# Performance work log

Hardware: AMD Instinct MI355X
Metric: run time of the kernel (lower is better)

Reference implementation:

```python
import jax, jax.numpy as jnp
import numpy as np

EPS = 1e-12

def _l2n(x):
    # torch F.normalize(p=2, dim=0): x / max(||x||_2, eps)
    return x / jnp.maximum(jnp.linalg.norm(x), EPS)

def _gru_cell(x, h, Wi, Wh, bi, bh):
    # torch GRU cell math; Wi:(3H,Din), Wh:(3H,H)
    gi = Wi @ x + bi
    gh = Wh @ h + bh
    i_r, i_z, i_n = jnp.split(gi, 3)
    h_r, h_z, h_n = jnp.split(gh, 3)
    r = jax.nn.sigmoid(i_r + h_r)
    z = jax.nn.sigmoid(i_z + h_z)
    n = jnp.tanh(i_n + r * h_n)
    return (1.0 - z) * n + z * h

def setup_inputs() -> dict:
    key = jax.random.key(0)
    ks = jax.random.split(key, 20)
    m, n, T = 10, 10, 100
    H1, H2, HID = 1600, 400, 2000
    D_in, D_out = 2 * m + n, m * n
    f32 = jnp.float32
    inp = {
        'y': jax.random.normal(ks[0], (n, T), f32),
        'm1x_0': jax.random.normal(ks[1], (m,), f32),
        'F': jax.random.normal(ks[2], (m, m), f32) * 0.1,
        'Hm': jax.random.normal(ks[3], (n, m), f32) * 0.1,
        'h0': jax.random.normal(ks[4], (2, HID), f32),
        'W1': jax.random.normal(ks[5], (H1, D_in), f32) * 0.05,
        'b1': jax.random.normal(ks[6], (H1,), f32) * 0.05,
        'Wi0': jax.random.normal(ks[7], (3 * HID, H1), f32) * 0.02,
        'Wh0': jax.random.normal(ks[8], (3 * HID, HID), f32) * 0.02,
        'bi0': jax.random.normal(ks[9], (3 * HID,), f32) * 0.02,
        'bh0': jax.random.normal(ks[10], (3 * HID,), f32) * 0.02,
        'Wi1': jax.random.normal(ks[11], (3 * HID, HID), f32) * 0.02,
        'Wh1': jax.random.normal(ks[12], (3 * HID, HID), f32) * 0.02,
        'bi1': jax.random.normal(ks[13], (3 * HID,), f32) * 0.02,
        'bh1': jax.random.normal(ks[14], (3 * HID,), f32) * 0.02,
        'W2': jax.random.normal(ks[15], (H2, HID), f32) * 0.02,
        'b2': jax.random.normal(ks[16], (H2,), f32) * 0.02,
        'W3': jax.random.normal(ks[17], (D_out, H2), f32) * 0.01,
        'b3': jax.random.normal(ks[18], (D_out,), f32) * 0.01,
    }
    return inp

def reference(y, m1x_0, F, Hm, h0, W1, b1, Wi0, Wh0, bi0, bh0,
              Wi1, Wh1, bi1, bh1, W2, b2, W3, b3):
    n, T = y.shape
    m = m1x_0.shape[0]
    # first step uses obs_process_0 = h(f(m1x_0)) as y_previous surrogate
    y_prev0 = Hm @ (F @ m1x_0)
    carry0 = (m1x_0, jnp.zeros_like(m1x_0), m1x_0, y_prev0, h0[0], h0[1])

    def step(carry, yt):
        post, prev_post, prev_prior, y_prev, h1, h2 = carry
        prior = F @ post              # step_prior
        m1y = Hm @ prior
        f1 = _l2n(yt - y_prev)        # innovation diff feature
        f3 = _l2n(post - prev_post)   # posterior update feature
        f4 = _l2n(post - prev_prior)  # residual feature
        kin = jnp.concatenate([f1, f3, f4])  # (2m+n,)
        a = jax.nn.relu(W1 @ kin + b1)
        h1n = _gru_cell(a, h1, Wi0, Wh0, bi0, bh0)
        h2n = _gru_cell(h1n, h2, Wi1, Wh1, bi1, bh1)
        g = jax.nn.relu(W2 @ h2n + b2)
        KG = (W3 @ g + b3).reshape(m, n)
        dy = yt - m1y
        new_post = prior + KG @ dy
        return (new_post, post, prior, yt, h1n, h2n), new_post

    _, xs = jax.lax.scan(step, carry0, y.T)  # xs: (T, m)
    return xs.T  # (m, T)
```

## Files before the change

### kernel.cpp

```cpp
#include <hip/hip_runtime.h>
#include <math.h>

#define NB 256
#define NT 1024
#define NW 16
#define TT 100
#define MM 10
#define NN 10
#define HID 2000
#define H1 1600
#define H2 400
#define G3 6000
#define KP 2048
#define RPB 24

#define SCOPE_AGENT __HIP_MEMORY_SCOPE_AGENT

typedef _Float16 h2v __attribute__((ext_vector_type(2)));

__device__ __forceinline__ float sigf(float x) { return 1.f / (1.f + __expf(-x)); }
__device__ __forceinline__ float tanhfast(float x) { return 2.f / (1.f + __expf(-2.f * x)) - 1.f; }

__device__ __forceinline__ float ld_coh(const float* p) {
  return __hip_atomic_load(p, __ATOMIC_RELAXED, SCOPE_AGENT);
}
__device__ __forceinline__ void st_coh(float* p, float v) {
  __hip_atomic_store(p, v, __ATOMIC_RELAXED, SCOPE_AGENT);
}
__device__ __forceinline__ float2 ld_coh2(const float* p) {
  unsigned long long v = __hip_atomic_load((const unsigned long long*)p,
                                           __ATOMIC_RELAXED, SCOPE_AGENT);
  union { unsigned long long u; float2 f; } c; c.u = v; return c.f;
}
__device__ __forceinline__ void stage_coh(const float* __restrict__ src,
                                          float* __restrict__ dst, int n, int tid) {
  const int n2 = n >> 1;
  for (int j = tid; j < n2; j += NT) {
    float2 v = ld_coh2(src + 2 * j);
    dst[2 * j]     = v.x;
    dst[2 * j + 1] = v.y;
  }
}

__device__ __forceinline__ void gridbar(unsigned* flags, unsigned* release,
                                        unsigned ep, int tid, int blk) {
  __syncthreads();
  if (tid == 0)
    __hip_atomic_store(flags + blk * 16, ep, __ATOMIC_RELAXED, SCOPE_AGENT);
  if (blk == 0) {
    if (tid < NB) {
      while (__hip_atomic_load(flags + tid * 16, __ATOMIC_RELAXED, SCOPE_AGENT) < ep)
        __builtin_amdgcn_s_sleep(1);
    }
    __syncthreads();
    if (tid == 0)
      __hip_atomic_store(release, ep, __ATOMIC_RELAXED, SCOPE_AGENT);
  } else {
    if (tid == 0) {
      while (__hip_atomic_load(release, __ATOMIC_RELAXED, SCOPE_AGENT) < ep)
        __builtin_amdgcn_s_sleep(1);
    }
  }
  __syncthreads();
}

template<int K>
__device__ __forceinline__ float rowdotT(const float* __restrict__ row,
                                         const float* __restrict__ x, int ln) {
  constexpr int NFULL = K / 256;
  constexpr int REM   = K - NFULL * 256;
  const int base = ln * 4;
  float4 w[NFULL + (REM ? 1 : 0)];
  #pragma unroll
  for (int i = 0; i < NFULL; ++i)
    w[i] = *reinterpret_cast<const float4*>(row + base + i * 256);
  bool tail = false;
  if constexpr (REM != 0) {
    tail = (base + NFULL * 256 + 3 < K);
    if (tail) w[NFULL] = *reinterpret_cast<const float4*>(row + base + NFULL * 256);
  }
  float acc = 0.f;
  #pragma unroll
  for (int i = 0; i < NFULL; ++i) {
    const float4 xv = *reinterpret_cast<const float4*>(x + base + i * 256);
    acc = fmaf(w[i].x, xv.x, acc);
    acc = fmaf(w[i].y, xv.y, acc);
    acc = fmaf(w[i].z, xv.z, acc);
    acc = fmaf(w[i].w, xv.w, acc);
  }
  if constexpr (REM != 0) {
    if (tail) {
      const float4 xv = *reinterpret_cast<const float4*>(x + base + NFULL * 256);
      acc = fmaf(w[NFULL].x, xv.x, acc);
      acc = fmaf(w[NFULL].y, xv.y, acc);
      acc = fmaf(w[NFULL].z, xv.z, acc);
      acc = fmaf(w[NFULL].w, xv.w, acc);
    }
  }
  #pragma unroll
  for (int off = 32; off; off >>= 1) acc += __shfl_xor(acc, off, 64);
  return acc;
}

__device__ __forceinline__ void sweep24(const _Float16* __restrict__ W,
                                        const float* __restrict__ bias,
                                        int row0, int nrows,
                                        const _Float16* __restrict__ xh,
                                        float* __restrict__ outw,
                                        bool relu,
                                        int wv, int ln, int tid, float* red)
{
  const _Float16* wp = W + (size_t)row0 * KP + wv * 3072 + ln * 8;
  uint4 w[6];
  #pragma unroll
  for (int c = 0; c < 6; ++c)
    w[c] = *reinterpret_cast<const uint4*>(wp + c * 512);
  float a0 = 0.f, a1 = 0.f;
  const int first = (3 * wv) >> 1;
  #pragma unroll
  for (int c = 0; c < 6; ++c) {
    const int flat = wv * 3072 + c * 512;
    const int sel  = (flat >> 11) - first;
    const int col  = (flat & (KP - 1)) + ln * 8;
    const uint4 xv = *reinterpret_cast<const uint4*>(xh + col);
    union { uint4 u; h2v h[4]; } wu, xu;
    wu.u = w[c]; xu.u = xv;
    float acc = sel ? a1 : a0;
    #pragma unroll
    for (int q = 0; q < 4; ++q)
      acc = __builtin_amdgcn_fdot2(wu.h[q], xu.h[q], acc, false);
    if (sel) a1 = acc; else a0 = acc;
  }
  #pragma unroll
  for (int off = 32; off; off >>= 1) {
    a0 += __shfl_xor(a0, off, 64);
    a1 += __shfl_xor(a1, off, 64);
  }
  __syncthreads();
  if (ln == 0) { red[wv * 2] = a0; red[wv * 2 + 1] = a1; }
  __syncthreads();
  if (tid < nrows) {
    const int k = tid / 3, m = tid % 3;
    float v = (m == 0) ? red[4 * k]
            : (m == 1) ? red[4 * k + 1] + red[4 * k + 2]
                       : red[4 * k + 3];
    v += bias[row0 + tid];
    if (relu) v = fmaxf(v, 0.f);
    st_coh(outw + row0 + tid, v);
  }
}

__global__ __launch_bounds__(256)
void convh(const float* __restrict__ src, _Float16* __restrict__ dst,
           int rows, int K, int padrows) {
  const size_t total = (size_t)padrows * KP;
  for (size_t i = (size_t)blockIdx.x * blockDim.x + threadIdx.x; i < total;
       i += (size_t)gridDim.x * blockDim.x) {
    const int r = (int)(i >> 11), c = (int)(i & (KP - 1));
    float v = (r < rows && c < K) ? src[(size_t)r * K + c] : 0.f;
    dst[i] = (_Float16)v;
  }
}

__global__ __launch_bounds__(NT)
void knet_f16(const float* __restrict__ y, const float* __restrict__ m1x0,
              const float* __restrict__ F, const float* __restrict__ Hm,
              const float* __restrict__ h0,
              const float* __restrict__ W1, const float* __restrict__ b1,
              const float* __restrict__ Wi0, const float* __restrict__ Wh0,
              const float* __restrict__ bi0, const float* __restrict__ bh0,
              const float* __restrict__ Wi1, const float* __restrict__ Wh1,
              const float* __restrict__ bi1, const float* __restrict__ bh1,
              const float* __restrict__ W2, const float* __restrict__ b2,
              const float* __restrict__ W3, const float* __restrict__ b3,
              float* __restrict__ out, float* __restrict__ ws)
{
  const int blk = blockIdx.x, tid = threadIdx.x;
  const int wv = tid >> 6, ln = tid & 63;

  float* a_ws   = ws;
  float* gi0_ws = ws + 1600;
  float* gh0_ws = ws + 7600;
  float* gi1_ws = ws + 13600;
  float* gh1_ws = ws + 19600;
  float* g_ws   = ws + 25600;
  unsigned* flags   = (unsigned*)(ws + 26624);
  unsigned* release = flags + NB * 16;

  const _Float16* whbase = (const _Float16*)((const char*)ws + 131072);
  const _Float16* Wi0h = whbase;
  const _Float16* Wh0h = whbase + (size_t)G3 * KP;
  const _Float16* Wi1h = whbase + (size_t)2 * G3 * KP;
  const _Float16* Wh1h = whbase + (size_t)3 * G3 * KP;
  const _Float16* W2h  = whbase + (size_t)4 * G3 * KP;

  __shared__ __align__(16) _Float16 ah[KP];
  __shared__ __align__(16) _Float16 h1h[KP];
  __shared__ __align__(16) _Float16 h2h[KP];
  __shared__ __align__(16) float h1l[HID];
  __shared__ __align__(16) float h2l[HID];
  __shared__ __align__(16) float xs[416];
  __shared__ float red[32];
  __shared__ float post_s[MM], prevpost_s[MM], prevprior_s[MM], prior_s[MM];
  __shared__ float dy_s[NN], yprev_s[NN], tmp_s[MM];
  __shared__ float d1_s[NN], d3_s[MM], d4_s[MM];
  __shared__ float kin_s[32], nrm_s[3];
  __shared__ float v_s[MM * NN], np_s[MM];

  for (int j = tid; j < HID; j += NT) {
    float v1 = h0[j], v2 = h0[HID + j];
    h1l[j] = v1; h2l[j] = v2;
    h1h[j] = (_Float16)v1; h2h[j] = (_Float16)v2;
  }
  for (int j = HID + tid; j < KP; j += NT) { h1h[j] = (_Float16)0.f; h2h[j] = (_Float16)0.f; }
  for (int j = H1 + tid; j < KP; j += NT) ah[j] = (_Float16)0.f;
  __syncthreads();

  unsigned ep = 0;

  for (int t = 0; t < TT; ++t) {
    if (blk == NB - 1) {
      if (t > 0) {
        stage_coh(g_ws, xs, H2, tid);
        __syncthreads();
        for (int r = wv; r < MM * NN; r += NW) {
          float acc = rowdotT<H2>(W3 + (size_t)r * H2, xs, ln);
          if (ln == 0) v_s[r] = acc + b3[r];
        }
        __syncthreads();
        if (tid < MM) {
          float np = prior_s[tid];
          #pragma unroll
          for (int j = 0; j < NN; ++j) np = fmaf(v_s[tid * NN + j], dy_s[j], np);
          out[tid * TT + (t - 1)] = np;
          np_s[tid] = np;
        }
        __syncthreads();
        if (tid < MM) {
          prevpost_s[tid]  = post_s[tid];
          prevprior_s[tid] = prior_s[tid];
          post_s[tid]      = np_s[tid];
        }
        __syncthreads();
      } else {
        if (tid < MM) {
          post_s[tid]      = m1x0[tid];
          prevpost_s[tid]  = 0.f;
          prevprior_s[tid] = m1x0[tid];
          float tv = 0.f;
          for (int j = 0; j < MM; ++j) tv = fmaf(F[tid * MM + j], m1x0[j], tv);
          tmp_s[tid] = tv;
        }
        __syncthreads();
        if (tid < NN) {
          float yp = 0.f;
          for (int j = 0; j < MM; ++j) yp = fmaf(Hm[tid * MM + j], tmp_s[j], yp);
          yprev_s[tid] = yp;
        }
        __syncthreads();
      }
      if (tid < MM) {
        float pr = 0.f;
        for (int j = 0; j < MM; ++j) pr = fmaf(F[tid * MM + j], post_s[j], pr);
        prior_s[tid] = pr;
      }
      __syncthreads();
      if (tid < NN) {
        float my = 0.f;
        for (int j = 0; j < MM; ++j) my = fmaf(Hm[tid * MM + j], prior_s[j], my);
        float yt = y[tid * TT + t];
        dy_s[tid] = yt - my;
        d1_s[tid] = yt - ((t == 0) ? yprev_s[tid] : y[tid * TT + (t - 1)]);
        d3_s[tid] = post_s[tid] - prevpost_s[tid];
        d4_s[tid] = post_s[tid] - prevprior_s[tid];
      }
      __syncthreads();
      if (tid == 0) {
        float n1 = 0.f, n3 = 0.f, n4 = 0.f;
        for (int j = 0; j < NN; ++j) n1 += d1_s[j] * d1_s[j];
        for (int j = 0; j < MM; ++j) { n3 += d3_s[j] * d3_s[j]; n4 += d4_s[j] * d4_s[j]; }
        nrm_s[0] = fmaxf(sqrtf(n1), 1e-12f);
        nrm_s[1] = fmaxf(sqrtf(n3), 1e-12f);
        nrm_s[2] = fmaxf(sqrtf(n4), 1e-12f);
      }
      __syncthreads();
      if (tid < NN) kin_s[tid] = d1_s[tid] / nrm_s[0];
      if (tid < MM) {
        kin_s[NN + tid]      = d3_s[tid] / nrm_s[1];
        kin_s[NN + MM + tid] = d4_s[tid] / nrm_s[2];
      }
      __syncthreads();
      for (int r = tid; r < H1; r += NT) {
        float acc = b1[r];
        const float* row = W1 + (size_t)r * 30;
        #pragma unroll
        for (int k = 0; k < 30; ++k) acc = fmaf(row[k], kin_s[k], acc);
        st_coh(a_ws + r, fmaxf(acc, 0.f));
      }
    } else if (blk < 250) {
      sweep24(Wh1h, bh1, RPB * blk, RPB, h2h, gh1_ws, false, wv, ln, tid, red);
      if (t == 0)
        sweep24(Wh0h, bh0, RPB * blk, RPB, h1h, gh0_ws, false, wv, ln, tid, red);
    } else {
      sweep24(Wh0h, bh0, RPB * (blk - 250), RPB, h1h, gh0_ws, false, wv, ln, tid, red);
    }
    ++ep; gridbar(flags, release, ep, tid, blk);

    if (blk < 250) {
      const int n2 = H1 >> 1;
      for (int j = tid; j < n2; j += NT) {
        float2 v = ld_coh2(a_ws + 2 * j);
        ah[2 * j]     = (_Float16)v.x;
        ah[2 * j + 1] = (_Float16)v.y;
      }
      __syncthreads();
      sweep24(Wi0h, bi0, RPB * blk, RPB, ah, gi0_ws, false, wv, ln, tid, red);
    } else {
      sweep24(Wh0h, bh0, RPB * (blk - 245), RPB, h1h, gh0_ws, false, wv, ln, tid, red);
    }
    ++ep; gridbar(flags, release, ep, tid, blk);

    {
      for (int j = tid; j < HID / 2; j += NT) {
        float2 ir = ld_coh2(gi0_ws + 2 * j),            hr = ld_coh2(gh0_ws + 2 * j);
        float2 iz = ld_coh2(gi0_ws + HID + 2 * j),      hz = ld_coh2(gh0_ws + HID + 2 * j);
        float2 in_ = ld_coh2(gi0_ws + 2 * HID + 2 * j), hn = ld_coh2(gh0_ws + 2 * HID + 2 * j);
        float r0 = sigf(ir.x + hr.x), r1 = sigf(ir.y + hr.y);
        float z0 = sigf(iz.x + hz.x), z1 = sigf(iz.y + hz.y);
        float n0 = tanhfast(in_.x + r0 * hn.x), n1 = tanhfast(in_.y + r1 * hn.y);
        float o0 = (1.f - z0) * n0 + z0 * h1l[2 * j];
        float o1 = (1.f - z1) * n1 + z1 * h1l[2 * j + 1];
        h1l[2 * j] = o0; h1l[2 * j + 1] = o1;
        h1h[2 * j] = (_Float16)o0; h1h[2 * j + 1] = (_Float16)o1;
      }
      __syncthreads();
      if (blk < 250)
        sweep24(Wi1h, bi1, RPB * blk, RPB, h1h, gi1_ws, false, wv, ln, tid, red);
    }
    ++ep; gridbar(flags, release, ep, tid, blk);

    {
      for (int j = tid; j < HID / 2; j += NT) {
        float2 ir = ld_coh2(gi1_ws + 2 * j),            hr = ld_coh2(gh1_ws + 2 * j);
        float2 iz = ld_coh2(gi1_ws + HID + 2 * j),      hz = ld_coh2(gh1_ws + HID + 2 * j);
        float2 in_ = ld_coh2(gi1_ws + 2 * HID + 2 * j), hn = ld_coh2(gh1_ws + 2 * HID + 2 * j);
        float r0 = sigf(ir.x + hr.x), r1 = sigf(ir.y + hr.y);
        float z0 = sigf(iz.x + hz.x), z1 = sigf(iz.y + hz.y);
        float n0 = tanhfast(in_.x + r0 * hn.x), n1 = tanhfast(in_.y + r1 * hn.y);
        float o0 = (1.f - z0) * n0 + z0 * h2l[2 * j];
        float o1 = (1.f - z1) * n1 + z1 * h2l[2 * j + 1];
        h2l[2 * j] = o0; h2l[2 * j + 1] = o1;
        h2h[2 * j] = (_Float16)o0; h2h[2 * j + 1] = (_Float16)o1;
      }
      __syncthreads();
      if (blk < 239) {
        sweep24(Wh0h, bh0, RPB * (blk + 11), RPB, h1h, gh0_ws, false, wv, ln, tid, red);
      } else {
        const int task = blk - 239;
        const int row0 = RPB * task;
        const int nr = (H2 - row0 < RPB) ? (H2 - row0) : RPB;
        sweep24(W2h, b2, row0, nr, h2h, g_ws, true, wv, ln, tid, red);
      }
    }
    ++ep; gridbar(flags, release, ep, tid, blk);
  }

  if (blk == NB - 1) {
    stage_coh(g_ws, xs, H2, tid);
    __syncthreads();
    for (int r = wv; r < MM * NN; r += NW) {
      float acc = rowdotT<H2>(W3 + (size_t)r * H2, xs, ln);
      if (ln == 0) v_s[r] = acc + b3[r];
    }
    __syncthreads();
    if (tid < MM) {
      float np = prior_s[tid];
      #pragma unroll
      for (int j = 0; j < NN; ++j) np = fmaf(v_s[tid * NN + j], dy_s[j], np);
      out[tid * TT + (TT - 1)] = np;
    }
  }
}

__global__ __launch_bounds__(NT)
void knet_f32(const float* __restrict__ y, const float* __restrict__ m1x0,
              const float* __restrict__ F, const float* __restrict__ Hm,
              const float* __restrict__ h0,
              const float* __restrict__ W1, const float* __restrict__ b1,
              const float* __restrict__ Wi0, const float* __restrict__ Wh0,
              const float* __restrict__ bi0, const float* __restrict__ bh0,
              const float* __restrict__ Wi1, const float* __restrict__ Wh1,
              const float* __restrict__ bi1, const float* __restrict__ bh1,
              const float* __restrict__ W2, const float* __restrict__ b2,
              const float* __restrict__ W3, const float* __restrict__ b3,
              float* __restrict__ out, float* __restrict__ ws)
{
  const int blk = blockIdx.x, tid = threadIdx.x;
  const int wv = tid >> 6, ln = tid & 63;

  float* a_ws   = ws;
  float* gi0_ws = ws + 1600;
  float* gh0_ws = ws + 7600;
  float* gi1_ws = ws + 13600;
  float* gh1_ws = ws + 19600;
  float* g_ws   = ws + 25600;
  unsigned* flags   = (unsigned*)(ws + 26624);
  unsigned* release = flags + NB * 16;

  __shared__ __align__(16) float xs[1664];
  __shared__ __align__(16) float h1l[HID];
  __shared__ __align__(16) float h2l[HID];
  __shared__ float post_s[MM], prevpost_s[MM], prevprior_s[MM], prior_s[MM];
  __shared__ float dy_s[NN], yprev_s[NN], tmp_s[MM];
  __shared__ float d1_s[NN], d3_s[MM], d4_s[MM];
  __shared__ float kin_s[32], nrm_s[3];
  __shared__ float v_s[MM * NN], np_s[MM];

  for (int j = tid; j < HID; j += NT) { h1l[j] = h0[j]; h2l[j] = h0[HID + j]; }
  __syncthreads();

  unsigned ep = 0;

  for (int t = 0; t < TT; ++t) {
    if (blk == NB - 1) {
      if (t > 0) {
        stage_coh(g_ws, xs, H2, tid);
        __syncthreads();
        for (int r = wv; r < MM * NN; r += NW) {
          float acc = rowdotT<H2>(W3 + (size_t)r * H2, xs, ln);
          if (ln == 0) v_s[r] = acc + b3[r];
        }
        __syncthreads();
        if (tid < MM) {
          float np = prior_s[tid];
          #pragma unroll
          for (int j = 0; j < NN; ++j) np = fmaf(v_s[tid * NN + j], dy_s[j], np);
          out[tid * TT + (t - 1)] = np;
          np_s[tid] = np;
        }
        __syncthreads();
        if (tid < MM) {
          prevpost_s[tid]  = post_s[tid];
          prevprior_s[tid] = prior_s[tid];
          post_s[tid]      = np_s[tid];
        }
        __syncthreads();
      } else {
        if (tid < MM) {
          post_s[tid]      = m1x0[tid];
          prevpost_s[tid]  = 0.f;
          prevprior_s[tid] = m1x0[tid];
          float tv = 0.f;
          for (int j = 0; j < MM; ++j) tv = fmaf(F[tid * MM + j], m1x0[j], tv);
          tmp_s[tid] = tv;
        }
        __syncthreads();
        if (tid < NN) {
          float yp = 0.f;
          for (int j = 0; j < MM; ++j) yp = fmaf(Hm[tid * MM + j], tmp_s[j], yp);
          yprev_s[tid] = yp;
        }
        __syncthreads();
      }
      if (tid < MM) {
        float pr = 0.f;
        for (int j = 0; j < MM; ++j) pr = fmaf(F[tid * MM + j], post_s[j], pr);
        prior_s[tid] = pr;
      }
      __syncthreads();
      if (tid < NN) {
        float my = 0.f;
        for (int j = 0; j < MM; ++j) my = fmaf(Hm[tid * MM + j], prior_s[j], my);
        float yt = y[tid * TT + t];
        dy_s[tid] = yt - my;
        d1_s[tid] = yt - ((t == 0) ? yprev_s[tid] : y[tid * TT + (t - 1)]);
        d3_s[tid] = post_s[tid] - prevpost_s[tid];
        d4_s[tid] = post_s[tid] - prevprior_s[tid];
      }
      __syncthreads();
      if (tid == 0) {
        float n1 = 0.f, n3 = 0.f, n4 = 0.f;
        for (int j = 0; j < NN; ++j) n1 += d1_s[j] * d1_s[j];
        for (int j = 0; j < MM; ++j) { n3 += d3_s[j] * d3_s[j]; n4 += d4_s[j] * d4_s[j]; }
        nrm_s[0] = fmaxf(sqrtf(n1), 1e-12f);
        nrm_s[1] = fmaxf(sqrtf(n3), 1e-12f);
        nrm_s[2] = fmaxf(sqrtf(n4), 1e-12f);
      }
      __syncthreads();
      if (tid < NN) kin_s[tid] = d1_s[tid] / nrm_s[0];
      if (tid < MM) {
        kin_s[NN + tid]      = d3_s[tid] / nrm_s[1];
        kin_s[NN + MM + tid] = d4_s[tid] / nrm_s[2];
      }
      __syncthreads();
      for (int r = tid; r < H1; r += NT) {
        float acc = b1[r];
        const float* row = W1 + (size_t)r * 30;
        #pragma unroll
        for (int k = 0; k < 30; ++k) acc = fmaf(row[k], kin_s[k], acc);
        st_coh(a_ws + r, fmaxf(acc, 0.f));
      }
    } else {
      const int gw = blk * NW + wv;
      for (int r = gw; r < G3; r += (NB - 1) * NW) {
        float acc = rowdotT<HID>(Wh1 + (size_t)r * HID, h2l, ln);
        if (ln == 0) st_coh(gh1_ws + r, acc + bh1[r]);
      }
      if (t == 0) {
        for (int r = gw; r < G3; r += (NB - 1) * NW) {
          float acc = rowdotT<HID>(Wh0 + (size_t)r * HID, h1l, ln);
          if (ln == 0) st_coh(gh0_ws + r, acc + bh0[r]);
        }
      }
    }
    ++ep; gridbar(flags, release, ep, tid, blk);

    stage_coh(a_ws, xs, H1, tid);
    __syncthreads();
    {
      const int gw = blk * NW + wv;
      for (int r = gw; r < G3; r += NB * NW) {
        float acc = rowdotT<H1>(Wi0 + (size_t)r * H1, xs, ln);
        if (ln == 0) st_coh(gi0_ws + r, acc + bi0[r]);
      }
    }
    ++ep; gridbar(flags, release, ep, tid, blk);

    {
      for (int j = tid; j < HID / 2; j += NT) {
        float2 ir = ld_coh2(gi0_ws + 2 * j),            hr = ld_coh2(gh0_ws + 2 * j);
        float2 iz = ld_coh2(gi0_ws + HID + 2 * j),      hz = ld_coh2(gh0_ws + HID + 2 * j);
        float2 in_ = ld_coh2(gi0_ws + 2 * HID + 2 * j), hn = ld_coh2(gh0_ws + 2 * HID + 2 * j);
        float r0 = sigf(ir.x + hr.x), r1 = sigf(ir.y + hr.y);
        float z0 = sigf(iz.x + hz.x), z1 = sigf(iz.y + hz.y);
        float n0 = tanhfast(in_.x + r0 * hn.x), n1 = tanhfast(in_.y + r1 * hn.y);
        h1l[2 * j]     = (1.f - z0) * n0 + z0 * h1l[2 * j];
        h1l[2 * j + 1] = (1.f - z1) * n1 + z1 * h1l[2 * j + 1];
      }
      __syncthreads();
      const int gw = blk * NW + wv;
      for (int r = gw; r < G3; r += NB * NW) {
        float acc = rowdotT<HID>(Wi1 + (size_t)r * HID, h1l, ln);
        if (ln == 0) st_coh(gi1_ws + r, acc + bi1[r]);
      }
    }
    ++ep; gridbar(flags, release, ep, tid, blk);

    {
      for (int j = tid; j < HID / 2; j += NT) {
        float2 ir = ld_coh2(gi1_ws + 2 * j),            hr = ld_coh2(gh1_ws + 2 * j);
        float2 iz = ld_coh2(gi1_ws + HID + 2 * j),      hz = ld_coh2(gh1_ws + HID + 2 * j);
        float2 in_ = ld_coh2(gi1_ws + 2 * HID + 2 * j), hn = ld_coh2(gh1_ws + 2 * HID + 2 * j);
        float r0 = sigf(ir.x + hr.x), r1 = sigf(ir.y + hr.y);
        float z0 = sigf(iz.x + hz.x), z1 = sigf(iz.y + hz.y);
        float n0 = tanhfast(in_.x + r0 * hn.x), n1 = tanhfast(in_.y + r1 * hn.y);
        h2l[2 * j]     = (1.f - z0) * n0 + z0 * h2l[2 * j];
        h2l[2 * j + 1] = (1.f - z1) * n1 + z1 * h2l[2 * j + 1];
      }
      __syncthreads();
      const int gw = blk * NW + wv;
      for (int r = gw; r < H2 + G3; r += NB * NW) {
        if (r < H2) {
          float acc = rowdotT<HID>(W2 + (size_t)r * HID, h2l, ln);
          if (ln == 0) st_coh(g_ws + r, fmaxf(acc + b2[r], 0.f));
        } else {
          const int rr = r - H2;
          float acc = rowdotT<HID>(Wh0 + (size_t)rr * HID, h1l, ln);
          if (ln == 0) st_coh(gh0_ws + rr, acc + bh0[rr]);
        }
      }
    }
    ++ep; gridbar(flags, release, ep, tid, blk);
  }

  if (blk == NB - 1) {
    stage_coh(g_ws, xs, H2, tid);
    __syncthreads();
    for (int r = wv; r < MM * NN; r += NW) {
      float acc = rowdotT<H2>(W3 + (size_t)r * H2, xs, ln);
      if (ln == 0) v_s[r] = acc + b3[r];
    }
    __syncthreads();
    if (tid < MM) {
      float np = prior_s[tid];
      #pragma unroll
      for (int j = 0; j < NN; ++j) np = fmaf(v_s[tid * NN + j], dy_s[j], np);
      out[tid * TT + (TT - 1)] = np;
    }
  }
}

extern "C" void kernel_launch(void* const* d_in, const int* in_sizes, int n_in,
                              void* d_out, int out_size, void* d_ws, size_t ws_size,
                              hipStream_t stream) {
  const float* y    = (const float*)d_in[0];
  const float* m1x0 = (const float*)d_in[1];
  const float* F    = (const float*)d_in[2];
  const float* Hm   = (const float*)d_in[3];
  const float* h0   = (const float*)d_in[4];
  const float* W1   = (const float*)d_in[5];
  const float* b1   = (const float*)d_in[6];
  const float* Wi0  = (const float*)d_in[7];
  const float* Wh0  = (const float*)d_in[8];
  const float* bi0  = (const float*)d_in[9];
  const float* bh0  = (const float*)d_in[10];
  const float* Wi1  = (const float*)d_in[11];
  const float* Wh1  = (const float*)d_in[12];
  const float* bi1  = (const float*)d_in[13];
  const float* bh1  = (const float*)d_in[14];
  const float* W2   = (const float*)d_in[15];
  const float* b2   = (const float*)d_in[16];
  const float* W3   = (const float*)d_in[17];
  const float* b3   = (const float*)d_in[18];
  float* out = (float*)d_out;
  float* ws  = (float*)d_ws;

  const size_t NEED = 131072 + ((size_t)4 * G3 * KP + 408 * KP) * 2;

  hipMemsetAsync((char*)d_ws + 26624 * sizeof(float), 0, NB * 64 + 64, stream);

  void* args[] = { &y, &m1x0, &F, &Hm, &h0, &W1, &b1, &Wi0, &Wh0, &bi0, &bh0,
                   &Wi1, &Wh1, &bi1, &bh1, &W2, &b2, &W3, &b3, &out, &ws };

  if (ws_size >= NEED) {
    _Float16* wh = (_Float16*)((char*)d_ws + 131072);
    convh<<<2048, 256, 0, stream>>>(Wi0, wh,                         G3, H1,  G3);
    convh<<<2048, 256, 0, stream>>>(Wh0, wh + (size_t)G3 * KP,       G3, HID, G3);
    convh<<<2048, 256, 0, stream>>>(Wi1, wh + (size_t)2 * G3 * KP,   G3, HID, G3);
    convh<<<2048, 256, 0, stream>>>(Wh1, wh + (size_t)3 * G3 * KP,   G3, HID, G3);
    convh<<<2048, 256, 0, stream>>>(W2,  wh + (size_t)4 * G3 * KP,   H2, HID, 408);
    hipLaunchCooperativeKernel((const void*)knet_f16, dim3(NB), dim3(NT),
                               args, 0, stream);
  } else {
    hipLaunchCooperativeKernel((const void*)knet_f32, dim3(NB), dim3(NT),
                               args, 0, stream);
  }
}
```

Baseline: 4.338 ms.

## Prefetch next weight tile across grid barriers and double-buffer gh0

Splits the f16 row sweep into a separate weight prefetch (pf6) and compute step, so each block loads the weights for its next phase into registers before entering the grid barrier. The custom barrier waits only partially on vector memory counters so those loads stay in flight across it. gh0 is double-buffered by timestep parity so Wh0 work can be spread over more phases, and the workspace layout is shifted to fit the second buffer. The cost is more register pressure and inline-asm waitcnt assumptions that could cause subtle ordering bugs; one call also contains an odd `gi0_ws == 0 ? 0 : gh0r` expression.

Result: slower. 5.167 ms (+19.1%).

```diff
diff --git a/kernel.cpp b/kernel.cpp
--- a/kernel.cpp
+++ b/kernel.cpp
@@ -42,17 +42,22 @@
   }
 }
 
-__device__ __forceinline__ void gridbar(unsigned* flags, unsigned* release,
-                                        unsigned ep, int tid, int blk) {
-  __syncthreads();
+__device__ __forceinline__ void gridbar2(unsigned* flags, unsigned* release,
+                                         unsigned ep, int tid, int blk) {
+  asm volatile("s_waitcnt vmcnt(6)" ::: "memory");
+  asm volatile("s_waitcnt lgkmcnt(0)" ::: "memory");
+  __builtin_amdgcn_sched_barrier(0);
+  __builtin_amdgcn_s_barrier();
+  __builtin_amdgcn_sched_barrier(0);
   if (tid == 0)
     __hip_atomic_store(flags + blk * 16, ep, __ATOMIC_RELAXED, SCOPE_AGENT);
+  __builtin_amdgcn_sched_barrier(0);
   if (blk == 0) {
     if (tid < NB) {
       while (__hip_atomic_load(flags + tid * 16, __ATOMIC_RELAXED, SCOPE_AGENT) < ep)
         __builtin_amdgcn_s_sleep(1);
     }
-    __syncthreads();
+    __builtin_amdgcn_s_barrier();
     if (tid == 0)
       __hip_atomic_store(release, ep, __ATOMIC_RELAXED, SCOPE_AGENT);
   } else {
@@ -61,7 +66,9 @@
         __builtin_amdgcn_s_sleep(1);
     }
   }
-  __syncthreads();
+  __builtin_amdgcn_sched_barrier(0);
+  __builtin_amdgcn_s_barrier();
+  __builtin_amdgcn_sched_barrier(0);
 }
 
 template<int K>
@@ -102,19 +109,21 @@
   return acc;
 }
 
-__device__ __forceinline__ void sweep24(const _Float16* __restrict__ W,
+__device__ __forceinline__ void pf6(const _Float16* __restrict__ W, int row0,
+                                    int wv, int ln, uint4* __restrict__ w) {
+  const _Float16* wp = W + (size_t)row0 * KP + wv * 3072 + ln * 8;
+  #pragma unroll
+  for (int c = 0; c < 6; ++c)
+    w[c] = *reinterpret_cast<const uint4*>(wp + c * 512);
+}
+
+__device__ __forceinline__ void sweep_c(const uint4* __restrict__ w,
                                         const float* __restrict__ bias,
                                         int row0, int nrows,
                                         const _Float16* __restrict__ xh,
-                                        float* __restrict__ outw,
-                                        bool relu,
+                                        float* __restrict__ outw, bool relu,
                                         int wv, int ln, int tid, float* red)
 {
-  const _Float16* wp = W + (size_t)row0 * KP + wv * 3072 + ln * 8;
-  uint4 w[6];
-  #pragma unroll
-  for (int c = 0; c < 6; ++c)
-    w[c] = *reinterpret_cast<const uint4*>(wp + c * 512);
   float a0 = 0.f, a1 = 0.f;
   const int first = (3 * wv) >> 1;
   #pragma unroll
@@ -181,13 +190,13 @@
   float* a_ws   = ws;
   float* gi0_ws = ws + 1600;
   float* gh0_ws = ws + 7600;
-  float* gi1_ws = ws + 13600;
-  float* gh1_ws = ws + 19600;
-  float* g_ws   = ws + 25600;
-  unsigned* flags   = (unsigned*)(ws + 26624);
+  float* gi1_ws = ws + 19600;
+  float* gh1_ws = ws + 25600;
+  float* g_ws   = ws + 31600;
+  unsigned* flags   = (unsigned*)(ws + 32000);
   unsigned* release = flags + NB * 16;
 
-  const _Float16* whbase = (const _Float16*)((const char*)ws + 131072);
+  const _Float16* whbase = (const _Float16*)((const char*)ws + 147456);
   const _Float16* Wi0h = whbase;
   const _Float16* Wh0h = whbase + (size_t)G3 * KP;
   const _Float16* Wi1h = whbase + (size_t)2 * G3 * KP;
@@ -216,9 +225,17 @@
   for (int j = H1 + tid; j < KP; j += NT) ah[j] = (_Float16)0.f;
   __syncthreads();
 
+  uint4 w6[6];
+  if (blk < 250)           pf6(Wh1h, RPB * blk, wv, ln, w6);
+  else if (blk < NB - 1)   pf6(Wh0h, RPB * (blk - 250), wv, ln, w6);
+  else                     pf6(Wh0h, RPB * 10, wv, ln, w6);
+
   unsigned ep = 0;
 
   for (int t = 0; t < TT; ++t) {
+    float* gh0r = gh0_ws + (t & 1) * G3;
+    float* gh0w = gh0_ws + ((t + 1) & 1) * G3;
+
     if (blk == NB - 1) {
       if (t > 0) {
         stage_coh(g_ws, xs, H2, tid);
@@ -297,14 +314,19 @@
         for (int k = 0; k < 30; ++k) acc = fmaf(row[k], kin_s[k], acc);
         st_coh(a_ws + r, fmaxf(acc, 0.f));
       }
+      pf6(Wh0h, RPB * 10, wv, ln, w6);
     } else if (blk < 250) {
-      sweep24(Wh1h, bh1, RPB * blk, RPB, h2h, gh1_ws, false, wv, ln, tid, red);
-      if (t == 0)
-        sweep24(Wh0h, bh0, RPB * blk, RPB, h1h, gh0_ws, false, wv, ln, tid, red);
+      sweep_c(w6, bh1, RPB * blk, RPB, h2h, gh1_ws, false, wv, ln, tid, red);
+      if (t == 0) {
+        pf6(Wh0h, RPB * blk, wv, ln, w6);
+        sweep_c(w6, bh0, RPB * blk, RPB, h1h, gh0r, false, wv, ln, tid, red);
+      }
+      pf6(Wi0h, RPB * blk, wv, ln, w6);
     } else {
-      sweep24(Wh0h, bh0, RPB * (blk - 250), RPB, h1h, gh0_ws, false, wv, ln, tid, red);
-    }
-    ++ep; gridbar(flags, release, ep, tid, blk);
+      sweep_c(w6, bh0, RPB * (blk - 250), RPB, h1h, gh0r, false, wv, ln, tid, red);
+      pf6(Wh0h, RPB * (blk - 245), wv, ln, w6);
+    }
+    ++ep; gridbar2(flags, release, ep, tid, blk);
 
     if (blk < 250) {
       const int n2 = H1 >> 1;
@@ -314,17 +336,22 @@
         ah[2 * j + 1] = (_Float16)v.y;
       }
       __syncthreads();
-      sweep24(Wi0h, bi0, RPB * blk, RPB, ah, gi0_ws, false, wv, ln, tid, red);
+      sweep_c(w6, bi0, RPB * blk, RPB, ah, gi0_ws, false, wv, ln, tid, red);
+      pf6(Wi1h, RPB * blk, wv, ln, w6);
+    } else if (blk < NB - 1) {
+      sweep_c(w6, bh0, RPB * (blk - 245), RPB, h1h, gi0_ws == 0 ? 0 : gh0r, false, wv, ln, tid, red);
+      pf6(Wh0h, RPB * (blk - 239), wv, ln, w6);
     } else {
-      sweep24(Wh0h, bh0, RPB * (blk - 245), RPB, h1h, gh0_ws, false, wv, ln, tid, red);
-    }
-    ++ep; gridbar(flags, release, ep, tid, blk);
+      sweep_c(w6, bh0, RPB * 10, RPB, h1h, gh0r, false, wv, ln, tid, red);
+      pf6(Wh0h, RPB * 16, wv, ln, w6);
+    }
+    ++ep; gridbar2(flags, release, ep, tid, blk);
 
     {
       for (int j = tid; j < HID / 2; j += NT) {
-        float2 ir = ld_coh2(gi0_ws + 2 * j),            hr = ld_coh2(gh0_ws + 2 * j);
-        float2 iz = ld_coh2(gi0_ws + HID + 2 * j),      hz = ld_coh2(gh0_ws + HID + 2 * j);
-        float2 in_ = ld_coh2(gi0_ws + 2 * HID + 2 * j), hn = ld_coh2(gh0_ws + 2 * HID + 2 * j);
+        float2 ir = ld_coh2(gi0_ws + 2 * j),            hr = ld_coh2(gh0r + 2 * j);
+        float2 iz = ld_coh2(gi0_ws + HID + 2 * j),      hz = ld_coh2(gh0r + HID + 2 * j);
+        float2 in_ = ld_coh2(gi0_ws + 2 * HID + 2 * j), hn = ld_coh2(gh0r + 2 * HID + 2 * j);
         float r0 = sigf(ir.x + hr.x), r1 = sigf(ir.y + hr.y);
         float z0 = sigf(iz.x + hz.x), z1 = sigf(iz.y + hz.y);
         float n0 = tanhfast(in_.x + r0 * hn.x), n1 = tanhfast(in_.y + r1 * hn.y);
@@ -334,10 +361,19 @@
         h1h[2 * j] = (_Float16)o0; h1h[2 * j + 1] = (_Float16)o1;
       }
       __syncthreads();
-      if (blk < 250)
-        sweep24(Wi1h, bi1, RPB * blk, RPB, h1h, gi1_ws, false, wv, ln, tid, red);
-    }
-    ++ep; gridbar(flags, release, ep, tid, blk);
+      if (blk < 250) {
+        sweep_c(w6, bi1, RPB * blk, RPB, h1h, gi1_ws, false, wv, ln, tid, red);
+        if (blk < 233) pf6(Wh0h, RPB * (blk + 17), wv, ln, w6);
+        else           pf6(W2h,  RPB * (blk - 233), wv, ln, w6);
+      } else if (blk < NB - 1) {
+        sweep_c(w6, bh0, RPB * (blk - 239), RPB, h1h, gh0w, false, wv, ln, tid, red);
+        pf6(Wh0h, RPB * (blk - 250), wv, ln, w6);
+      } else {
+        sweep_c(w6, bh0, RPB * 16, RPB, h1h, gh0w, false, wv, ln, tid, red);
+        pf6(Wh0h, RPB * 10, wv, ln, w6);
+      }
+    }
+    ++ep; gridbar2(flags, release, ep, tid, blk);
 
     {
       for (int j = tid; j < HID / 2; j += NT) {
@@ -353,16 +389,17 @@
         h2h[2 * j] = (_Float16)o0; h2h[2 * j + 1] = (_Float16)o1;
       }
       __syncthreads();
-      if (blk < 239) {
-        sweep24(Wh0h, bh0, RPB * (blk + 11), RPB, h1h, gh0_ws, false, wv, ln, tid, red);
-      } else {
-        const int task = blk - 239;
-        const int row0 = RPB * task;
+      if (blk < 233) {
+        sweep_c(w6, bh0, RPB * (blk + 17), RPB, h1h, gh0w, false, wv, ln, tid, red);
+        pf6(Wh1h, RPB * blk, wv, ln, w6);
+      } else if (blk < 250) {
+        const int row0 = RPB * (blk - 233);
         const int nr = (H2 - row0 < RPB) ? (H2 - row0) : RPB;
-        sweep24(W2h, b2, row0, nr, h2h, g_ws, true, wv, ln, tid, red);
-      }
-    }
-    ++ep; gridbar(flags, release, ep, tid, blk);
+        sweep_c(w6, b2, row0, nr, h2h, g_ws, true, wv, ln, tid, red);
+        pf6(Wh1h, RPB * blk, wv, ln, w6);
+      }
+    }
+    ++ep; gridbar2(flags, release, ep, tid, blk);
   }
 
   if (blk == NB - 1) {
@@ -380,6 +417,28 @@
       out[tid * TT + (TT - 1)] = np;
     }
   }
+}
+
+__device__ __forceinline__ void gridbar(unsigned* flags, unsigned* release,
+                                        unsigned ep, int tid, int blk) {
+  __syncthreads();
+  if (tid == 0)
+    __hip_atomic_store(flags + blk * 16, ep, __ATOMIC_RELAXED, SCOPE_AGENT);
+  if (blk == 0) {
+    if (tid < NB) {
+      while (__hip_atomic_load(flags + tid * 16, __ATOMIC_RELAXED, SCOPE_AGENT) < ep)
+        __builtin_amdgcn_s_sleep(1);
+    }
+    __syncthreads();
+    if (tid == 0)
+      __hip_atomic_store(release, ep, __ATOMIC_RELAXED, SCOPE_AGENT);
+  } else {
+    if (tid == 0) {
+      while (__hip_atomic_load(release, __ATOMIC_RELAXED, SCOPE_AGENT) < ep)
+        __builtin_amdgcn_s_sleep(1);
+    }
+  }
+  __syncthreads();
 }
 
 __global__ __launch_bounds__(NT)
@@ -604,10 +663,10 @@
   const float* Wh0  = (const float*)d_in[8];
   const float* bi0  = (const float*)d_in[9];
   const float* bh0  = (const float*)d_in[10];
+  const float* bh1  = (const float*)d_in[14];
   const float* Wi1  = (const float*)d_in[11];
   const float* Wh1  = (const float*)d_in[12];
   const float* bi1  = (const float*)d_in[13];
-  const float* bh1  = (const float*)d_in[14];
   const float* W2   = (const float*)d_in[15];
   const float* b2   = (const float*)d_in[16];
   const float* W3   = (const float*)d_in[17];
@@ -615,15 +674,14 @@
   float* out = (float*)d_out;
   float* ws  = (float*)d_ws;
 
-  const size_t NEED = 131072 + ((size_t)4 * G3 * KP + 408 * KP) * 2;
-
-  hipMemsetAsync((char*)d_ws + 26624 * sizeof(float), 0, NB * 64 + 64, stream);
+  const size_t NEED = 147456 + ((size_t)4 * G3 * KP + (size_t)408 * KP) * 2;
 
   void* args[] = { &y, &m1x0, &F, &Hm, &h0, &W1, &b1, &Wi0, &Wh0, &bi0, &bh0,
                    &Wi1, &Wh1, &bi1, &bh1, &W2, &b2, &W3, &b3, &out, &ws };
 
   if (ws_size >= NEED) {
-    _Float16* wh = (_Float16*)((char*)d_ws + 131072);
+    hipMemsetAsync((char*)d_ws + 128000, 0, NB * 64 + 64, stream);
+    _Float16* wh = (_Float16*)((char*)d_ws + 147456);
     convh<<<2048, 256, 0, stream>>>(Wi0, wh,                         G3, H1,  G3);
     convh<<<2048, 256, 0, stream>>>(Wh0, wh + (size_t)G3 * KP,       G3, HID, G3);
     convh<<<2048, 256, 0, stream>>>(Wi1, wh + (size_t)2 * G3 * KP,   G3, HID, G3);
@@ -632,6 +690,7 @@
     hipLaunchCooperativeKernel((const void*)knet_f16, dim3(NB), dim3(NT),
                                args, 0, stream);
   } else {
+    hipMemsetAsync((char*)d_ws + 26624 * sizeof(float), 0, NB * 64 + 64, stream);
     hipLaunchCooperativeKernel((const void*)knet_f32, dim3(NB), dim3(NT),
                                args, 0, stream);
   }
```

## Distribute W3 projection into W2 sweep blocks and use f16 dot for W1

Applied to the files above, without the earlier changes.

The W3 output projection is split across the blocks that compute W2 rows. Each of those blocks multiplies its local ReLU outputs by the matching W3 columns and writes partial sums, and the last block only adds 17 partials per output. This takes the serial 100x400 matvec off the critical path of that block at each step. W1 is also converted to padded f16, and the first layer uses packed fdot2 with 800 threads handling two rows each, which changes precision slightly.

New measurement: 3.760 ms. -13.3%, faster.

```diff
diff --git a/kernel.cpp b/kernel.cpp
--- a/kernel.cpp
+++ b/kernel.cpp
@@ -108,7 +108,8 @@
                                         const _Float16* __restrict__ xh,
                                         float* __restrict__ outw,
                                         bool relu,
-                                        int wv, int ln, int tid, float* red)
+                                        int wv, int ln, int tid, float* red,
+                                        float* __restrict__ gloc)
 {
   const _Float16* wp = W + (size_t)row0 * KP + wv * 3072 + ln * 8;
   uint4 w[6];
@@ -146,6 +147,7 @@
                        : red[4 * k + 3];
     v += bias[row0 + tid];
     if (relu) v = fmaxf(v, 0.f);
+    if (gloc) gloc[tid] = v;
     st_coh(outw + row0 + tid, v);
   }
 }
@@ -160,6 +162,13 @@
     float v = (r < rows && c < K) ? src[(size_t)r * K + c] : 0.f;
     dst[i] = (_Float16)v;
   }
+}
+__global__ __launch_bounds__(256)
+void convw1(const float* __restrict__ src, _Float16* __restrict__ dst) {
+  const int i = blockIdx.x * 256 + threadIdx.x;
+  const int r = i >> 5, c = i & 31;
+  float v = (r < H1 && c < 30) ? src[r * 30 + c] : 0.f;
+  dst[i] = (_Float16)v;
 }
 
 __global__ __launch_bounds__(NT)
@@ -178,13 +187,14 @@
   const int blk = blockIdx.x, tid = threadIdx.x;
   const int wv = tid >> 6, ln = tid & 63;
 
-  float* a_ws   = ws;
-  float* gi0_ws = ws + 1600;
-  float* gh0_ws = ws + 7600;
-  float* gi1_ws = ws + 13600;
-  float* gh1_ws = ws + 19600;
-  float* g_ws   = ws + 25600;
-  unsigned* flags   = (unsigned*)(ws + 26624);
+  float* a_ws    = ws;
+  float* gi0_ws  = ws + 1600;
+  float* gh0_ws  = ws + 7600;
+  float* gi1_ws  = ws + 13600;
+  float* gh1_ws  = ws + 19600;
+  float* g_ws    = ws + 25600;
+  float* vpart_ws = ws + 26000;
+  unsigned* flags   = (unsigned*)(ws + 27712);
   unsigned* release = flags + NB * 16;
 
   const _Float16* whbase = (const _Float16*)((const char*)ws + 131072);
@@ -193,14 +203,17 @@
   const _Float16* Wi1h = whbase + (size_t)2 * G3 * KP;
   const _Float16* Wh1h = whbase + (size_t)3 * G3 * KP;
   const _Float16* W2h  = whbase + (size_t)4 * G3 * KP;
+  const _Float16* W1h  = whbase + (size_t)4 * G3 * KP + (size_t)408 * KP;
 
   __shared__ __align__(16) _Float16 ah[KP];
   __shared__ __align__(16) _Float16 h1h[KP];
   __shared__ __align__(16) _Float16 h2h[KP];
   __shared__ __align__(16) float h1l[HID];
   __shared__ __align__(16) float h2l[HID];
-  __shared__ __align__(16) float xs[416];
+  __shared__ __align__(16) float xs[1728];
+  __shared__ __align__(16) _Float16 kin_h[32];
   __shared__ float red[32];
+  __shared__ float gloc_s[RPB];
   __shared__ float post_s[MM], prevpost_s[MM], prevprior_s[MM], prior_s[MM];
   __shared__ float dy_s[NN], yprev_s[NN], tmp_s[MM];
   __shared__ float d1_s[NN], d3_s[MM], d4_s[MM];
@@ -221,11 +234,13 @@
   for (int t = 0; t < TT; ++t) {
     if (blk == NB - 1) {
       if (t > 0) {
-        stage_coh(g_ws, xs, H2, tid);
-        __syncthreads();
-        for (int r = wv; r < MM * NN; r += NW) {
-          float acc = rowdotT<H2>(W3 + (size_t)r * H2, xs, ln);
-          if (ln == 0) v_s[r] = acc + b3[r];
+        stage_coh(vpart_ws, xs, 1700, tid);
+        __syncthreads();
+        if (tid < MM * NN) {
+          float s = b3[tid];
+          #pragma unroll
+          for (int k = 0; k < 17; ++k) s += xs[k * 100 + tid];
+          v_s[tid] = s;
         }
         __syncthreads();
         if (tid < MM) {
@@ -290,19 +305,44 @@
         kin_s[NN + MM + tid] = d4_s[tid] / nrm_s[2];
       }
       __syncthreads();
-      for (int r = tid; r < H1; r += NT) {
-        float acc = b1[r];
-        const float* row = W1 + (size_t)r * 30;
+      if (tid < 32) kin_h[tid] = (_Float16)((tid < 30) ? kin_s[tid] : 0.f);
+      __syncthreads();
+      if (tid < 800) {
+        const _Float16* wp = W1h + (size_t)tid * 64;
+        uint4 q[8];
         #pragma unroll
-        for (int k = 0; k < 30; ++k) acc = fmaf(row[k], kin_s[k], acc);
-        st_coh(a_ws + r, fmaxf(acc, 0.f));
+        for (int c = 0; c < 8; ++c)
+          q[c] = *reinterpret_cast<const uint4*>(wp + c * 8);
+        const uint4* kq = reinterpret_cast<const uint4*>(kin_h);
+        union { uint4 u; h2v h[4]; } kk[4], qq;
+        #pragma unroll
+        for (int c = 0; c < 4; ++c) kk[c].u = kq[c];
+        const int r0 = 2 * tid;
+        float s0 = b1[r0], s1 = b1[r0 + 1];
+        #pragma unroll
+        for (int c = 0; c < 4; ++c) {
+          qq.u = q[c];
+          #pragma unroll
+          for (int p = 0; p < 4; ++p)
+            s0 = __builtin_amdgcn_fdot2(qq.h[p], kk[c].h[p], s0, false);
+        }
+        #pragma unroll
+        for (int c = 0; c < 4; ++c) {
+          qq.u = q[c + 4];
+          #pragma unroll
+          for (int p = 0; p < 4; ++p)
+            s1 = __builtin_amdgcn_fdot2(qq.h[p], kk[c].h[p], s1, false);
+        }
+        st_coh(a_ws + r0,     fmaxf(s0, 0.f));
+        st_coh(a_ws + r0 + 1, fmaxf(s1, 0.f));
       }
     } else if (blk < 250) {
-      sweep24(Wh1h, bh1, RPB * blk, RPB, h2h, gh1_ws, false, wv, ln, tid, red);
-      if (t == 0)
-        sweep24(Wh0h, bh0, RPB * blk, RPB, h1h, gh0_ws, false, wv, ln, tid, red);
+      sweep24(Wh1h, bh1, RPB * blk, RPB, h2h, gh1_ws, false, wv, ln, tid, red, nullptr);
+      if (t == 0) {
+        sweep24(Wh0h, bh0, RPB * blk, RPB, h1h, gh0_ws, false, wv, ln, tid, red, nullptr);
+      }
     } else {
-      sweep24(Wh0h, bh0, RPB * (blk - 250), RPB, h1h, gh0_ws, false, wv, ln, tid, red);
+      sweep24(Wh0h, bh0, RPB * (blk - 250), RPB, h1h, gh0_ws, false, wv, ln, tid, red, nullptr);
     }
     ++ep; gridbar(flags, release, ep, tid, blk);
 
@@ -314,9 +354,9 @@
         ah[2 * j + 1] = (_Float16)v.y;
       }
       __syncthreads();
-      sweep24(Wi0h, bi0, RPB * blk, RPB, ah, gi0_ws, false, wv, ln, tid, red);
+      sweep24(Wi0h, bi0, RPB * blk, RPB, ah, gi0_ws, false, wv, ln, tid, red, nullptr);
     } else {
-      sweep24(Wh0h, bh0, RPB * (blk - 245), RPB, h1h, gh0_ws, false, wv, ln, tid, red);
+      sweep24(Wh0h, bh0, RPB * (blk - 245), RPB, h1h, gh0_ws, false, wv, ln, tid, red, nullptr);
     }
     ++ep; gridbar(flags, release, ep, tid, blk);
 
@@ -335,7 +375,7 @@
       }
       __syncthreads();
       if (blk < 250)
-        sweep24(Wi1h, bi1, RPB * blk, RPB, h1h, gi1_ws, false, wv, ln, tid, red);
+        sweep24(Wi1h, bi1, RPB * blk, RPB, h1h, gi1_ws, false, wv, ln, tid, red, nullptr);
     }
     ++ep; gridbar(flags, release, ep, tid, blk);
 
@@ -354,23 +394,32 @@
       }
       __syncthreads();
       if (blk < 239) {
-        sweep24(Wh0h, bh0, RPB * (blk + 11), RPB, h1h, gh0_ws, false, wv, ln, tid, red);
+        sweep24(Wh0h, bh0, RPB * (blk + 11), RPB, h1h, gh0_ws, false, wv, ln, tid, red, nullptr);
       } else {
         const int task = blk - 239;
         const int row0 = RPB * task;
         const int nr = (H2 - row0 < RPB) ? (H2 - row0) : RPB;
-        sweep24(W2h, b2, row0, nr, h2h, g_ws, true, wv, ln, tid, red);
+        sweep24(W2h, b2, row0, nr, h2h, g_ws, true, wv, ln, tid, red, gloc_s);
+        __syncthreads();
+        if (tid < MM * NN) {
+          float s = 0.f;
+          const float* w3c = W3 + (size_t)tid * H2 + row0;
+          for (int j = 0; j < nr; ++j) s = fmaf(w3c[j], gloc_s[j], s);
+          st_coh(vpart_ws + task * 100 + tid, s);
+        }
       }
     }
     ++ep; gridbar(flags, release, ep, tid, blk);
   }
 
   if (blk == NB - 1) {
-    stage_coh(g_ws, xs, H2, tid);
+    stage_coh(vpart_ws, xs, 1700, tid);
     __syncthreads();
-    for (int r = wv; r < MM * NN; r += NW) {
-      float acc = rowdotT<H2>(W3 + (size_t)r * H2, xs, ln);
-      if (ln == 0) v_s[r] = acc + b3[r];
+    if (tid < MM * NN) {
+      float s = b3[tid];
+      #pragma unroll
+      for (int k = 0; k < 17; ++k) s += xs[k * 100 + tid];
+      v_s[tid] = s;
     }
     __syncthreads();
     if (tid < MM) {
@@ -615,23 +664,25 @@
   float* out = (float*)d_out;
   float* ws  = (float*)d_ws;
 
-  const size_t NEED = 131072 + ((size_t)4 * G3 * KP + 408 * KP) * 2;
-
-  hipMemsetAsync((char*)d_ws + 26624 * sizeof(float), 0, NB * 64 + 64, stream);
+  const size_t NEED = 131072 +
+      ((size_t)4 * G3 * KP + (size_t)408 * KP + (size_t)65536) * 2;
 
   void* args[] = { &y, &m1x0, &F, &Hm, &h0, &W1, &b1, &Wi0, &Wh0, &bi0, &bh0,
                    &Wi1, &Wh1, &bi1, &bh1, &W2, &b2, &W3, &b3, &out, &ws };
 
   if (ws_size >= NEED) {
+    hipMemsetAsync((char*)d_ws + 110848, 0, NB * 64 + 64, stream);
     _Float16* wh = (_Float16*)((char*)d_ws + 131072);
     convh<<<2048, 256, 0, stream>>>(Wi0, wh,                         G3, H1,  G3);
     convh<<<2048, 256, 0, stream>>>(Wh0, wh + (size_t)G3 * KP,       G3, HID, G3);
     convh<<<2048, 256, 0, stream>>>(Wi1, wh + (size_t)2 * G3 * KP,   G3, HID, G3);
     convh<<<2048, 256, 0, stream>>>(Wh1, wh + (size_t)3 * G3 * KP,   G3, HID, G3);
     convh<<<2048, 256, 0, stream>>>(W2,  wh + (size_t)4 * G3 * KP,   H2, HID, 408);
+    convw1<<<256, 256, 0, stream>>>(W1,  wh + (size_t)4 * G3 * KP + (size_t)408 * KP);
     hipLaunchCooperativeKernel((const void*)knet_f16, dim3(NB), dim3(NT),
                                args, 0, stream);
   } else {
+    hipMemsetAsync((char*)d_ws + 26624 * sizeof(float), 0, NB * 64 + 64, stream);
     hipLaunchCooperativeKernel((const void*)knet_f32, dim3(NB), dim3(NT),
                                args, 0, stream);
   }
```
